# Optimization experiments

Measured on AMD Instinct MI355X. Metric: run time of the kernel, lower is better.

## Reference

```python
import jax, jax.numpy as jnp
import numpy as np

SIGMA = 0.2
BN_EPS = 1e-5


def setup_inputs() -> dict:
    key = jax.random.key(0)
    k1, k2, k3, k4 = jax.random.split(key, 4)
    B, F, K, M = 8, 16384, 3, 64
    normals = jax.random.normal(k1, (B, 3, F), dtype=jnp.float32)
    # normalize to unit vectors (face normals), keeps math well-conditioned
    normals = normals / jnp.linalg.norm(normals, axis=1, keepdims=True)
    weight_alpha = jax.random.uniform(k2, (1, M, 4), dtype=jnp.float32) * np.pi
    weight_beta = jax.random.uniform(k3, (1, M, 4), dtype=jnp.float32) * 2 * np.pi
    bn_gamma = jnp.ones((M,), dtype=jnp.float32)
    bn_beta = jnp.zeros((M,), dtype=jnp.float32)
    neighbor_index = jax.random.randint(k4, (B, F, K), 0, F, dtype=jnp.int64)
    return {"normals": normals, "weight_alpha": weight_alpha,
            "weight_beta": weight_beta, "bn_gamma": bn_gamma,
            "bn_beta": bn_beta, "neighbor_index": neighbor_index}


def reference(normals, weight_alpha, weight_beta, bn_gamma, bn_beta, neighbor_index):
    # normals: [B, 3, F]; neighbor_index: [B, F, K]
    B, _, F = normals.shape
    K = neighbor_index.shape[-1]
    # kernel points on unit sphere from spherical angles: [3, M, 4]
    sa, ca = jnp.sin(weight_alpha), jnp.cos(weight_alpha)
    sb, cb = jnp.sin(weight_beta), jnp.cos(weight_beta)
    w = jnp.concatenate([sa * cb, sa * sb, ca], axis=0)  # [3, M, 4]

    nt = jnp.transpose(normals, (0, 2, 1))  # [B, F, 3]
    # gather neighbor normals per batch: [B, F, K, 3]
    neigh = jax.vmap(lambda n, idx: n[idx])(nt, neighbor_index)
    # points per face: center + K neighbors -> [B, F, K+1, 3]
    pts = jnp.concatenate([nt[:, :, None, :], neigh], axis=2)

    # squared distance via expansion: ||p||^2 + ||w||^2 - 2 p.w
    dot = jnp.einsum('bfic,cmj->bmfij', pts, w)        # [B, M, F, K+1, 4]
    p2 = jnp.sum(pts * pts, axis=-1)                   # [B, F, K+1]
    w2 = jnp.sum(w * w, axis=0)                        # [M, 4]
    dist = (p2[:, None, :, :, None] + w2[None, :, None, None, :] - 2.0 * dot)

    feat = jnp.sum(jnp.exp(dist / (-2.0 * SIGMA ** 2)), axis=(3, 4))
    feat = feat / float((K + 1) * 4)                   # [B, M, F]

    # BatchNorm1d (training-mode batch stats over B and F per channel M)
    mean = jnp.mean(feat, axis=(0, 2), keepdims=True)
    var = jnp.var(feat, axis=(0, 2), keepdims=True)
    xhat = (feat - mean) / jnp.sqrt(var + BN_EPS)
    out = xhat * bn_gamma[None, :, None] + bn_beta[None, :, None]
    return jax.nn.relu(out)
```

## Files before the change

kernel.cpp:

```cpp
#include <hip/hip_runtime.h>

#define B_DIM 8
#define F_DIM 16384
#define K_DIM 3
#define M_DIM 64
#define MCH   16
#define LOG2E 1.4426950408889634f

#define WS_Q 32768
#define WS_W 65536

__global__ void fkc_wtab_kernel(const float* __restrict__ walpha,
                                const float* __restrict__ wbeta,
                                float* __restrict__ ws)
{
    const int t = threadIdx.x;
    float a = walpha[t], b = wbeta[t];
    float sa = sinf(a), ca = cosf(a);
    float sb = sinf(b), cb = cosf(b);
    float wx = sa * cb, wy = sa * sb, wz = ca;
    float w2 = wx * wx + wy * wy + wz * wz;
    ((float4*)(ws + WS_W))[t] =
        make_float4(wx * 25.0f * LOG2E, wy * 25.0f * LOG2E,
                    wz * 25.0f * LOG2E, -12.5f * LOG2E * (w2 + 1.0f));
}

__global__ __launch_bounds__(256) void fkc_feat_kernel(
    const float*  __restrict__ normals,
    const int*    __restrict__ nidx,
    const float4* __restrict__ wtab,
    float* __restrict__ feat_out,
    float* __restrict__ ws)
{
    __shared__ float4 sW[MCH * 4];
    __shared__ float sRS[MCH][64];
    __shared__ float sRQ[MCH][64];

    const int tid = threadIdx.x;
    const int b  = blockIdx.x >> 8;
    const int mc = (blockIdx.x >> 6) & 3;
    const int fc = blockIdx.x & 63;

    if (tid < MCH * 4) sW[tid] = wtab[mc * MCH * 4 + tid];
    __syncthreads();

    const int f = (fc << 8) + tid;
    const float* nb = normals + (size_t)b * 3 * F_DIM;
    float px[4], py[4], pz[4];
    px[0] = nb[f]; py[0] = nb[F_DIM + f]; pz[0] = nb[2 * F_DIM + f];
    const int* ib = nidx + ((size_t)b * F_DIM + f) * K_DIM;
#pragma unroll
    for (int k = 0; k < K_DIM; ++k) {
        int id = ib[k];
        px[k + 1] = nb[id]; py[k + 1] = nb[F_DIM + id]; pz[k + 1] = nb[2 * F_DIM + id];
    }

    const int wave = tid >> 6, lane = tid & 63;
    float* outb = feat_out + ((size_t)b * M_DIM + mc * MCH) * F_DIM + f;
#pragma unroll 2
    for (int m = 0; m < MCH; ++m) {
        float s0 = 0.f, s1 = 0.f, s2 = 0.f, s3 = 0.f;
#pragma unroll
        for (int j = 0; j < 4; ++j) {
            float4 w = sW[m * 4 + j];
            s0 += __builtin_amdgcn_exp2f(fmaf(w.x, px[0], fmaf(w.y, py[0], fmaf(w.z, pz[0], w.w))));
            s1 += __builtin_amdgcn_exp2f(fmaf(w.x, px[1], fmaf(w.y, py[1], fmaf(w.z, pz[1], w.w))));
            s2 += __builtin_amdgcn_exp2f(fmaf(w.x, px[2], fmaf(w.y, py[2], fmaf(w.z, pz[2], w.w))));
            s3 += __builtin_amdgcn_exp2f(fmaf(w.x, px[3], fmaf(w.y, py[3], fmaf(w.z, pz[3], w.w))));
        }
        float S = (s0 + s1) + (s2 + s3);
        outb[(size_t)m * F_DIM] = S;

        float s = S, q = S * S;
        s += __shfl_xor(s, 16, 64); q += __shfl_xor(q, 16, 64);
        s += __shfl_xor(s, 32, 64); q += __shfl_xor(q, 32, 64);
        if (lane < 16) { sRS[m][wave * 16 + lane] = s; sRQ[m][wave * 16 + lane] = q; }
    }
    __syncthreads();

    {
        const int m = tid >> 4, j = tid & 15;
        float s = (sRS[m][j] + sRS[m][j + 16]) + (sRS[m][j + 32] + sRS[m][j + 48]);
        float q = (sRQ[m][j] + sRQ[m][j + 16]) + (sRQ[m][j + 32] + sRQ[m][j + 48]);
        s += __shfl_xor(s, 1, 64);  q += __shfl_xor(q, 1, 64);
        s += __shfl_xor(s, 2, 64);  q += __shfl_xor(q, 2, 64);
        s += __shfl_xor(s, 4, 64);  q += __shfl_xor(q, 4, 64);
        s += __shfl_xor(s, 8, 64);  q += __shfl_xor(q, 8, 64);
        if (j == 0) {
            int slot = (mc * MCH + m) * 512 + b * 64 + fc;
            ws[slot] = s;
            ws[WS_Q + slot] = q;
        }
    }
}

__global__ __launch_bounds__(256) void fkc_bn_kernel(
    float* __restrict__ out,
    const float* __restrict__ gamma,
    const float* __restrict__ beta,
    const float* __restrict__ ws)
{
    __shared__ float sS[4], sQ[4];
    __shared__ float sAC[2];
    const int row = blockIdx.x;
    const int m = row & 63;
    const int tid = threadIdx.x;
    const int wave = tid >> 6, lane = tid & 63;

    {
        float s = ws[m * 512 + tid]        + ws[m * 512 + tid + 256];
        float q = ws[WS_Q + m * 512 + tid] + ws[WS_Q + m * 512 + tid + 256];
#pragma unroll
        for (int off = 32; off >= 1; off >>= 1) {
            s += __shfl_xor(s, off, 64);
            q += __shfl_xor(q, off, 64);
        }
        if (lane == 0) { sS[wave] = s; sQ[wave] = q; }
    }
    __syncthreads();
    if (tid == 0) {
        float s = (sS[0] + sS[1]) + (sS[2] + sS[3]);
        float q = (sQ[0] + sQ[1]) + (sQ[2] + sQ[3]);
        const float invcnt = 1.0f / (float)(B_DIM * F_DIM);
        float meanS = s * invcnt;
        float meanF = meanS * (1.0f / 16.0f);
        float ef2   = q * invcnt * (1.0f / 256.0f);
        float var   = ef2 - meanF * meanF;
        float inv   = rsqrtf(var + 1e-5f);
        float A = gamma[m] * inv;
        sAC[0] = A * (1.0f / 16.0f);
        sAC[1] = beta[m] - meanF * A;
    }
    __syncthreads();

    const float A = sAC[0], C = sAC[1];
    float4* p4 = (float4*)(out + (size_t)row * F_DIM);
#pragma unroll
    for (int i = 0; i < 16; ++i) {
        float4 v = p4[tid + i * 256];
        v.x = fmaxf(fmaf(v.x, A, C), 0.0f);
        v.y = fmaxf(fmaf(v.y, A, C), 0.0f);
        v.z = fmaxf(fmaf(v.z, A, C), 0.0f);
        v.w = fmaxf(fmaf(v.w, A, C), 0.0f);
        p4[tid + i * 256] = v;
    }
}

extern "C" void kernel_launch(void* const* d_in, const int* in_sizes, int n_in,
                              void* d_out, int out_size, void* d_ws, size_t ws_size,
                              hipStream_t stream)
{
    const float* normals = (const float*)d_in[0];
    const float* walpha  = (const float*)d_in[1];
    const float* wbeta   = (const float*)d_in[2];
    const float* gamma   = (const float*)d_in[3];
    const float* beta    = (const float*)d_in[4];
    const int*   nidx    = (const int*)d_in[5];
    float* out = (float*)d_out;
    float* ws  = (float*)d_ws;

    hipLaunchKernelGGL(fkc_wtab_kernel, dim3(1), dim3(256), 0, stream,
                       walpha, wbeta, ws);
    hipLaunchKernelGGL(fkc_feat_kernel, dim3(2048), dim3(256), 0, stream,
                       normals, nidx, (const float4*)(ws + WS_W), out, ws);
    hipLaunchKernelGGL(fkc_bn_kernel, dim3(B_DIM * M_DIM), dim3(256), 0, stream,
                       out, gamma, beta, ws);
}
```

Measured before the change: 54.93 us.

## Fuse weight-table prep into feature kernel, use readlane weights and LDS-transposed stats

Removes the separate single-block weight-table kernel: each feature block now computes its own 16 kernel points (sin/cos) into shared memory. The inner loop pulls weights into scalar registers with readlane from one VGPR per chunk instead of LDS float4 reads. The per-channel sum and sum-of-squares reduction now stages feature values in a padded LDS tile and reduces row-wise, replacing the per-m shuffle reductions. This trades one kernel launch plus per-iteration shuffles and LDS reads for redundant trig work in every block and a larger shared-memory footprint.

Result: faster. 53.81 us (-2.0%).

```diff
diff --git a/kernel.cpp b/kernel.cpp
--- a/kernel.cpp
+++ b/kernel.cpp
@@ -4,44 +4,41 @@
 #define F_DIM 16384
 #define K_DIM 3
 #define M_DIM 64
-#define MCH   16
 #define LOG2E 1.4426950408889634f
 
 #define WS_Q 32768
-#define WS_W 65536
 
-__global__ void fkc_wtab_kernel(const float* __restrict__ walpha,
-                                const float* __restrict__ wbeta,
-                                float* __restrict__ ws)
-{
-    const int t = threadIdx.x;
-    float a = walpha[t], b = wbeta[t];
-    float sa = sinf(a), ca = cosf(a);
-    float sb = sinf(b), cb = cosf(b);
-    float wx = sa * cb, wy = sa * sb, wz = ca;
-    float w2 = wx * wx + wy * wy + wz * wz;
-    ((float4*)(ws + WS_W))[t] =
-        make_float4(wx * 25.0f * LOG2E, wy * 25.0f * LOG2E,
-                    wz * 25.0f * LOG2E, -12.5f * LOG2E * (w2 + 1.0f));
-}
+#define WGET(TV, I) __int_as_float(__builtin_amdgcn_readlane(__float_as_int(TV), (I)))
 
 __global__ __launch_bounds__(256) void fkc_feat_kernel(
-    const float*  __restrict__ normals,
-    const int*    __restrict__ nidx,
-    const float4* __restrict__ wtab,
+    const float* __restrict__ normals,
+    const float* __restrict__ walpha,
+    const float* __restrict__ wbeta,
+    const int*   __restrict__ nidx,
     float* __restrict__ feat_out,
     float* __restrict__ ws)
 {
-    __shared__ float4 sW[MCH * 4];
-    __shared__ float sRS[MCH][64];
-    __shared__ float sRQ[MCH][64];
+    __shared__ float sWf[256];
+    __shared__ float T[16 * 257];
+    __shared__ float sBS[16][4], sBQ[16][4];
 
     const int tid = threadIdx.x;
     const int b  = blockIdx.x >> 8;
     const int mc = (blockIdx.x >> 6) & 3;
     const int fc = blockIdx.x & 63;
 
-    if (tid < MCH * 4) sW[tid] = wtab[mc * MCH * 4 + tid];
+    if (tid < 64) {
+        int idx = mc * 64 + tid;
+        float a = walpha[idx], bb = wbeta[idx];
+        float sa = sinf(a), ca = cosf(a);
+        float sb = sinf(bb), cb = cosf(bb);
+        float wx = sa * cb, wy = sa * sb, wz = ca;
+        float w2 = wx * wx + wy * wy + wz * wz;
+        sWf[tid * 4 + 0] = wx * 25.0f * LOG2E;
+        sWf[tid * 4 + 1] = wy * 25.0f * LOG2E;
+        sWf[tid * 4 + 2] = wz * 25.0f * LOG2E;
+        sWf[tid * 4 + 3] = -12.5f * LOG2E * (w2 + 1.0f);
+    }
     __syncthreads();
 
     const int f = (fc << 8) + tid;
@@ -55,42 +52,54 @@
         px[k + 1] = nb[id]; py[k + 1] = nb[F_DIM + id]; pz[k + 1] = nb[2 * F_DIM + id];
     }
 
-    const int wave = tid >> 6, lane = tid & 63;
-    float* outb = feat_out + ((size_t)b * M_DIM + mc * MCH) * F_DIM + f;
-#pragma unroll 2
-    for (int m = 0; m < MCH; ++m) {
-        float s0 = 0.f, s1 = 0.f, s2 = 0.f, s3 = 0.f;
+    const int lane = tid & 63;
+    float* outb = feat_out + ((size_t)b * M_DIM + mc * 16) * F_DIM + f;
+
+#pragma unroll 1
+    for (int c = 0; c < 4; ++c) {
+        float tv = sWf[c * 64 + lane];
 #pragma unroll
-        for (int j = 0; j < 4; ++j) {
-            float4 w = sW[m * 4 + j];
-            s0 += __builtin_amdgcn_exp2f(fmaf(w.x, px[0], fmaf(w.y, py[0], fmaf(w.z, pz[0], w.w))));
-            s1 += __builtin_amdgcn_exp2f(fmaf(w.x, px[1], fmaf(w.y, py[1], fmaf(w.z, pz[1], w.w))));
-            s2 += __builtin_amdgcn_exp2f(fmaf(w.x, px[2], fmaf(w.y, py[2], fmaf(w.z, pz[2], w.w))));
-            s3 += __builtin_amdgcn_exp2f(fmaf(w.x, px[3], fmaf(w.y, py[3], fmaf(w.z, pz[3], w.w))));
+        for (int ms = 0; ms < 4; ++ms) {
+            float s0 = 0.f, s1 = 0.f, s2 = 0.f, s3 = 0.f;
+#pragma unroll
+            for (int j = 0; j < 4; ++j) {
+                const int base = ms * 16 + j * 4;
+                float wx = WGET(tv, base + 0);
+                float wy = WGET(tv, base + 1);
+                float wz = WGET(tv, base + 2);
+                float ww = WGET(tv, base + 3);
+                asm("" : "+v"(ww));
+                s0 += __builtin_amdgcn_exp2f(fmaf(wx, px[0], fmaf(wy, py[0], fmaf(wz, pz[0], ww))));
+                s1 += __builtin_amdgcn_exp2f(fmaf(wx, px[1], fmaf(wy, py[1], fmaf(wz, pz[1], ww))));
+                s2 += __builtin_amdgcn_exp2f(fmaf(wx, px[2], fmaf(wy, py[2], fmaf(wz, pz[2], ww))));
+                s3 += __builtin_amdgcn_exp2f(fmaf(wx, px[3], fmaf(wy, py[3], fmaf(wz, pz[3], ww))));
+            }
+            float S = (s0 + s1) + (s2 + s3);
+            const int m = c * 4 + ms;
+            outb[(size_t)m * F_DIM] = S;
+            T[m * 257 + tid] = S;
         }
-        float S = (s0 + s1) + (s2 + s3);
-        outb[(size_t)m * F_DIM] = S;
-
-        float s = S, q = S * S;
-        s += __shfl_xor(s, 16, 64); q += __shfl_xor(q, 16, 64);
-        s += __shfl_xor(s, 32, 64); q += __shfl_xor(q, 32, 64);
-        if (lane < 16) { sRS[m][wave * 16 + lane] = s; sRQ[m][wave * 16 + lane] = q; }
     }
     __syncthreads();
 
     {
-        const int m = tid >> 4, j = tid & 15;
-        float s = (sRS[m][j] + sRS[m][j + 16]) + (sRS[m][j + 32] + sRS[m][j + 48]);
-        float q = (sRQ[m][j] + sRQ[m][j + 16]) + (sRQ[m][j + 32] + sRQ[m][j + 48]);
-        s += __shfl_xor(s, 1, 64);  q += __shfl_xor(q, 1, 64);
-        s += __shfl_xor(s, 2, 64);  q += __shfl_xor(q, 2, 64);
-        s += __shfl_xor(s, 4, 64);  q += __shfl_xor(q, 4, 64);
-        s += __shfl_xor(s, 8, 64);  q += __shfl_xor(q, 8, 64);
-        if (j == 0) {
-            int slot = (mc * MCH + m) * 512 + b * 64 + fc;
-            ws[slot] = s;
-            ws[WS_Q + slot] = q;
-        }
+        const int m = tid & 15, jj = tid >> 4;
+        const float* row = &T[m * 257 + jj * 16];
+        float s = 0.f, q = 0.f;
+#pragma unroll
+        for (int i = 0; i < 16; ++i) { float v = row[i]; s += v; q = fmaf(v, v, q); }
+        s += __shfl_xor(s, 16, 64); q += __shfl_xor(q, 16, 64);
+        s += __shfl_xor(s, 32, 64); q += __shfl_xor(q, 32, 64);
+        const int wave = tid >> 6;
+        if ((tid & 48) == 0) { sBS[m][wave] = s; sBQ[m][wave] = q; }
+    }
+    __syncthreads();
+    if (tid < 16) {
+        float s = (sBS[tid][0] + sBS[tid][1]) + (sBS[tid][2] + sBS[tid][3]);
+        float q = (sBQ[tid][0] + sBQ[tid][1]) + (sBQ[tid][2] + sBQ[tid][3]);
+        int slot = (mc * 16 + tid) * 512 + b * 64 + fc;
+        ws[slot] = s;
+        ws[WS_Q + slot] = q;
     }
 }
 
@@ -159,10 +168,8 @@
     float* out = (float*)d_out;
     float* ws  = (float*)d_ws;
 
-    hipLaunchKernelGGL(fkc_wtab_kernel, dim3(1), dim3(256), 0, stream,
-                       walpha, wbeta, ws);
     hipLaunchKernelGGL(fkc_feat_kernel, dim3(2048), dim3(256), 0, stream,
-                       normals, nidx, (const float4*)(ws + WS_W), out, ws);
+                       normals, walpha, wbeta, nidx, out, ws);
     hipLaunchKernelGGL(fkc_bn_kernel, dim3(B_DIM * M_DIM), dim3(256), 0, stream,
                        out, gamma, beta, ws);
 }
```
